# Kernel tuning notes

Measured on AMD Instinct MI355X. Metric: run time of the kernel, lower is better.

The kernel has to match this reference:

```python
import jax, jax.numpy as jnp
import numpy as np

B, L, C, D, H, NB, K = 8, 1024, 4, 64, 8, 2, 16  # batch, seq, conds, dim, heads, blocks, rbf centers

def _ln(x, s, b):
    m = x.mean(-1, keepdims=True)
    v = x.var(-1, keepdims=True)
    return (x - m) / jnp.sqrt(v + 1e-6) * s + b

def setup_inputs() -> dict:
    key = jax.random.key(0)
    ks = jax.random.split(key, 24)
    rn = lambda i, shape, sc=0.02: jax.random.normal(ks[i], shape, jnp.float32) * sc
    inp = {}
    inp['z'] = jax.random.normal(ks[0], (B, L), jnp.float32)
    inp['conditionals'] = jax.random.normal(ks[1], (C,), jnp.float32)
    inp['s'] = jnp.sort(jax.random.uniform(ks[2], (L,), jnp.float32))
    inp['embed'] = rn(3, (L, 2 * D - (C + 1)))  # positional id embedding table
    # input MLP([4D, D]) with gelu
    inp['Win1'] = rn(4, (2 * D, 4 * D)); inp['bin1'] = jnp.zeros((4 * D,), jnp.float32)
    inp['Win2'] = rn(5, (4 * D, D));     inp['bin2'] = jnp.zeros((D,), jnp.float32)
    # per-block (leading dim NB) transformer params
    inp['ln1_s'] = jnp.ones((NB, D), jnp.float32); inp['ln1_b'] = jnp.zeros((NB, D), jnp.float32)
    inp['ln2_s'] = jnp.ones((NB, D), jnp.float32); inp['ln2_b'] = jnp.zeros((NB, D), jnp.float32)
    inp['Wq'] = rn(6, (NB, D, 2 * D)); inp['bq'] = jnp.zeros((NB, 2 * D), jnp.float32)
    inp['Wk'] = rn(7, (NB, D, 2 * D)); inp['bk'] = jnp.zeros((NB, 2 * D), jnp.float32)
    inp['Wv'] = rn(8, (NB, D, 2 * D)); inp['bv'] = jnp.zeros((NB, 2 * D), jnp.float32)
    inp['Wo'] = rn(9, (NB, 2 * D, D)); inp['bo'] = jnp.zeros((NB, D), jnp.float32)
    # RBF-network attention bias: features exp(-(d-c)^2/(2w^2)) -> linear to H heads
    inp['rbf_c'] = jnp.tile(jnp.linspace(-1.0, 1.0, K, dtype=jnp.float32)[None], (NB, 1))
    inp['rbf_logw'] = jnp.full((NB, K), -1.0, jnp.float32)
    inp['rbf_w'] = rn(10, (NB, K, H), 0.1); inp['rbf_b'] = jnp.zeros((NB, H), jnp.float32)
    # FFN MLP([4D, D])
    inp['W1'] = rn(11, (NB, D, 4 * D)); inp['b1'] = jnp.zeros((NB, 4 * D), jnp.float32)
    inp['W2'] = rn(12, (NB, 4 * D, D)); inp['b2'] = jnp.zeros((NB, D), jnp.float32)
    # head MLP([4D, D, 1])
    inp['Wh1'] = rn(13, (D, 4 * D)); inp['bh1'] = jnp.zeros((4 * D,), jnp.float32)
    inp['Wh2'] = rn(14, (4 * D, D)); inp['bh2'] = jnp.zeros((D,), jnp.float32)
    inp['Wh3'] = rn(15, (D, 1));     inp['bh3'] = jnp.zeros((1,), jnp.float32)
    return inp

def reference(z, conditionals, s, embed, Win1, bin1, Win2, bin2,
              ln1_s, ln1_b, ln2_s, ln2_b, Wq, bq, Wk, bk, Wv, bv, Wo, bo,
              rbf_c, rbf_logw, rbf_w, rbf_b, W1, b1, W2, b2,
              Wh1, bh1, Wh2, bh2, Wh3, bh3):
    Bn, Ln = z.shape
    Cn = conditionals.shape[0]
    Hn = rbf_w.shape[-1]
    dh = Wq.shape[-1] // Hn
    scale = 1.0 / jnp.sqrt(jnp.float32(dh))
    # cond_as_feats: [z, broadcast conditionals] -> (B, L, C+1); prepend ids embedding -> (B, L, 2D)
    feats = jnp.concatenate([
        jnp.broadcast_to(embed[None], (Bn,) + embed.shape),
        z[..., None],
        jnp.broadcast_to(conditionals[None, None, :], (Bn, Ln, Cn)),
    ], axis=-1)
    x = jax.nn.gelu(feats @ Win1 + bin1) @ Win2 + bin2  # (B, L, D)
    dist = s[:, None] - s[None, :]  # (L, L) pairwise query-key coordinate diff (same per batch)
    for i in range(Wq.shape[0]):
        h = _ln(x, ln1_s[i], ln1_b[i])
        q = (h @ Wq[i] + bq[i]).reshape(Bn, Ln, Hn, dh)
        k = (h @ Wk[i] + bk[i]).reshape(Bn, Ln, Hn, dh)
        v = (h @ Wv[i] + bv[i]).reshape(Bn, Ln, Hn, dh)
        scores = jnp.einsum('bqhd,bkhd->bhqk', q, k) * scale
        # RBF-network bias on pairwise distances, per head
        phi = jnp.exp(-(dist[..., None] - rbf_c[i]) ** 2 / (2.0 * jnp.exp(rbf_logw[i]) ** 2))  # (L, L, K)
        bias = jnp.einsum('qkf,fh->hqk', phi, rbf_w[i]) + rbf_b[i][:, None, None]  # (H, L, L)
        a = jax.nn.softmax(scores + bias[None], axis=-1)
        o = jnp.einsum('bhqk,bkhd->bqhd', a, v).reshape(Bn, Ln, Hn * dh)
        x = x + o @ Wo[i] + bo[i]
        h2 = _ln(x, ln2_s[i], ln2_b[i])
        x = x + jax.nn.gelu(h2 @ W1[i] + b1[i]) @ W2[i] + b2[i]
    hh = jax.nn.gelu(x @ Wh1 + bh1)
    hh = jax.nn.gelu(hh @ Wh2 + bh2)
    return hh @ Wh3 + bh3  # f_hat: (B, L, 1)
```

## Files before the change

kernel.cpp:

```cpp
#include <hip/hip_runtime.h>
#include <hip/hip_bf16.h>

#define BB   8
#define LL   1024
#define DD   64
#define D2   128
#define D4   256
#define HH   8
#define DH   16

typedef __attribute__((ext_vector_type(8))) short short8;
typedef __attribute__((ext_vector_type(4))) float floatx4;

#define OFF_WIN1   0
#define OFF_WIN2   65536
#define OFF_LAY0   98304
#define LAY_STRIDE 131072
#define OFF_WQ     0
#define OFF_WK     16384
#define OFF_WV     32768
#define OFF_WO     49152
#define OFF_W1     65536
#define OFF_W2     98304
#define OFF_WH1    360448
#define OFF_WH2    393216

__device__ __forceinline__ float gelu_tanh(float u) {
  float t = tanhf(0.7978845608028654f * (u + 0.044715f * u * u * u));
  return 0.5f * u * (1.0f + t);
}

__device__ __forceinline__ float wave_reduce_sum(float v) {
#pragma unroll
  for (int m = 32; m >= 1; m >>= 1) v += __shfl_xor(v, m, 64);
  return v;
}

__device__ __forceinline__ unsigned short f2bf(float x) {
  unsigned u = __float_as_uint(x);
  u += 0x7fffu + ((u >> 16) & 1u);
  return (unsigned short)(u >> 16);
}

__device__ __forceinline__ float bf2f(unsigned short x) {
  return __uint_as_float(((unsigned)x) << 16);
}

__device__ __forceinline__ void split_bf(float v, unsigned short& hi,
                                         unsigned short& lo) {
  hi = f2bf(v);
  lo = f2bf(v - bf2f(hi));
}

template <int K, int KP>
__device__ __forceinline__ floatx4 mfma_tile(
    const unsigned short* Ah, const unsigned short* Al,
    const unsigned short* __restrict__ Bh, const unsigned short* __restrict__ Bl,
    int lq, int quad, floatx4 C) {
#pragma unroll
  for (int kk = 0; kk < K; kk += 32) {
    short8 ah = *(const short8*)(Ah + lq * KP + kk + quad * 8);
    short8 al = *(const short8*)(Al + lq * KP + kk + quad * 8);
    short8 bh = *(const short8*)(Bh + lq * K + kk + quad * 8);
    short8 bl = *(const short8*)(Bl + lq * K + kk + quad * 8);
    C = __builtin_amdgcn_mfma_f32_16x16x32_bf16(ah, bh, C, 0, 0, 0);
    C = __builtin_amdgcn_mfma_f32_16x16x32_bf16(al, bh, C, 0, 0, 0);
    C = __builtin_amdgcn_mfma_f32_16x16x32_bf16(ah, bl, C, 0, 0, 0);
  }
  return C;
}

struct PrepArgs {
  const float* src[16];
  int Kd[16], Nd[16], dst[16], elems[16];
};

__global__ __launch_bounds__(256) void k_prep(PrepArgs a,
                                              unsigned short* __restrict__ arena) {
  int mid = blockIdx.y;
  int e = blockIdx.x * 256 + threadIdx.x;
  int KN = a.elems[mid];
  if (e >= KN) return;
  int K = a.Kd[mid], N = a.Nd[mid];
  int n = e / K, k = e - n * K;
  float wv = a.src[mid][k * N + n];
  unsigned short hi, lo;
  split_bf(wv, hi, lo);
  arena[a.dst[mid] + e] = hi;
  arena[a.dst[mid] + KN + e] = lo;
}

__global__ __launch_bounds__(256) void k_bias(
    const float* __restrict__ s, const float* __restrict__ rbf_c,
    const float* __restrict__ rbf_logw, const float* __restrict__ rbf_w,
    const float* __restrict__ rbf_b, unsigned short* __restrict__ biasT) {
  int lay = blockIdx.y;
  int id = blockIdx.x * 256 + threadIdx.x;
  int q = id >> 10, k = id & 1023;
  float dd = s[q] - s[k];
  float acc[8];
#pragma unroll
  for (int h = 0; h < 8; ++h) acc[h] = rbf_b[lay * 8 + h];
#pragma unroll 1
  for (int f = 0; f < 16; ++f) {
    float c = rbf_c[lay * 16 + f];
    float inv2w2 = 0.5f * __expf(-2.0f * rbf_logw[lay * 16 + f]);
    float e = dd - c;
    float ph = __expf(-e * e * inv2w2);
#pragma unroll
    for (int h = 0; h < 8; ++h)
      acc[h] = fmaf(ph, rbf_w[lay * 128 + f * 8 + h], acc[h]);
  }
  unsigned short* bT = biasT + (size_t)lay * 8 * 1024 * 1024;
#pragma unroll
  for (int h = 0; h < 8; ++h)
    bT[(size_t)(h * 1024 + q) * 1024 + k] = f2bf(acc[h]);
}

__device__ __forceinline__ void qkv_tail(
    const float* xl, unsigned short* Sh, unsigned short* Sl,
    const unsigned short* __restrict__ arena, int lay,
    const float* __restrict__ ln_s, const float* __restrict__ ln_b,
    const float* __restrict__ bq, const float* __restrict__ bk,
    const float* __restrict__ bv, unsigned short* __restrict__ qo,
    unsigned short* __restrict__ ko, unsigned short* __restrict__ voT,
    int tok0, int t) {
  int w = t >> 6, lane = t & 63;
  int lq = lane & 15, quad = lane >> 4;
  float ss = ln_s[lay * 64 + lane], sb = ln_b[lay * 64 + lane];
#pragma unroll
  for (int tk = 0; tk < 4; ++tk) {
    int tok = w * 4 + tk;
    float v = xl[tok * 64 + lane];
    float mean = wave_reduce_sum(v) * 0.015625f;
    float d = v - mean;
    float var = wave_reduce_sum(d * d) * 0.015625f;
    float hv = d * rsqrtf(var + 1e-6f) * ss + sb;
    unsigned short hi, lo;
    split_bf(hv, hi, lo);
    Sh[tok * 72 + lane] = hi;
    Sl[tok * 72 + lane] = lo;
  }
  __syncthreads();
  int b = tok0 >> 10, l0 = tok0 & 1023;
#pragma unroll 1
  for (int mat = 0; mat < 3; ++mat) {
    const unsigned short* Bh =
        arena + OFF_LAY0 + lay * LAY_STRIDE + mat * 16384;
    const unsigned short* Bl = Bh + 8192;
    const float* bias = (mat == 0 ? bq : mat == 1 ? bk : bv) + lay * 128;
#pragma unroll
    for (int j = 0; j < 2; ++j) {
      int tl = w + j * 4;
      int n = tl * 16 + lq;
      float bb = bias[n];
      floatx4 C = {bb, bb, bb, bb};
      C = mfma_tile<64, 72>(Sh, Sl, Bh + tl * 16 * 64, Bl + tl * 16 * 64,
                            lq, quad, C);
      if (mat < 2) {
        unsigned short* outp = (mat == 0 ? qo : ko);
        size_t basea = ((size_t)(b * 8 + tl) * 1024 + l0 + quad * 4) * 16 + lq;
#pragma unroll
        for (int r = 0; r < 4; ++r)
          outp[basea + (size_t)r * 16] = f2bf(C[r]);
      } else {
        size_t basev = ((size_t)(b * 8 + tl) * 16 + lq) * 1024 + l0 + quad * 4;
#pragma unroll
        for (int r = 0; r < 4; ++r)
          voT[basev + r] = f2bf(C[r]);
      }
    }
  }
}

__global__ __launch_bounds__(256) void k_in_qkv(
    const float* __restrict__ embed, const float* __restrict__ z,
    const float* __restrict__ cond, const unsigned short* __restrict__ arena,
    const float* __restrict__ bin1, const float* __restrict__ bin2,
    float* __restrict__ x, const float* __restrict__ ln1_s,
    const float* __restrict__ ln1_b, const float* __restrict__ bq,
    const float* __restrict__ bk, const float* __restrict__ bv,
    unsigned short* __restrict__ qo, unsigned short* __restrict__ ko,
    unsigned short* __restrict__ voT) {
  __shared__ __align__(16) unsigned short Ah[16 * 136], Al[16 * 136];
  __shared__ __align__(16) unsigned short Hh[16 * 264], Hl[16 * 264];
  __shared__ __align__(16) unsigned short Sh[16 * 72], Sl[16 * 72];
  __shared__ float xl[16 * 64];
  int t = threadIdx.x, w = t >> 6, lane = t & 63;
  int lq = lane & 15, quad = lane >> 4;
  int tok0 = blockIdx.x * 16;
  for (int idx = t; idx < 2048; idx += 256) {
    int tok = idx >> 7, dim = idx & 127;
    int bl = tok0 + tok, l = bl & (LL - 1);
    float v;
    if (dim < 123) v = embed[l * 123 + dim];
    else if (dim == 123) v = z[bl];
    else v = cond[dim - 124];
    unsigned short hi, lo;
    split_bf(v, hi, lo);
    Ah[tok * 136 + dim] = hi;
    Al[tok * 136 + dim] = lo;
  }
  __syncthreads();
  const unsigned short* B1h = arena + OFF_WIN1;
  const unsigned short* B1l = B1h + 32768;
#pragma unroll
  for (int j = 0; j < 4; ++j) {
    int tl = w * 4 + j, n = tl * 16 + lq;
    float bb = bin1[n];
    floatx4 C = {bb, bb, bb, bb};
    C = mfma_tile<128, 136>(Ah, Al, B1h + tl * 16 * 128, B1l + tl * 16 * 128,
                            lq, quad, C);
#pragma unroll
    for (int r = 0; r < 4; ++r) {
      float g = gelu_tanh(C[r]);
      unsigned short hi, lo;
      split_bf(g, hi, lo);
      Hh[(quad * 4 + r) * 264 + n] = hi;
      Hl[(quad * 4 + r) * 264 + n] = lo;
    }
  }
  __syncthreads();
  const unsigned short* B2h = arena + OFF_WIN2;
  const unsigned short* B2l = B2h + 16384;
  {
    int n = w * 16 + lq;
    float bb = bin2[n];
    floatx4 C = {bb, bb, bb, bb};
    C = mfma_tile<256, 264>(Hh, Hl, B2h + w * 16 * 256, B2l + w * 16 * 256,
                            lq, quad, C);
#pragma unroll
    for (int r = 0; r < 4; ++r) {
      int m = quad * 4 + r;
      x[(size_t)(tok0 + m) * 64 + n] = C[r];
      xl[m * 64 + n] = C[r];
    }
  }
  __syncthreads();
  qkv_tail(xl, Sh, Sl, arena, 0, ln1_s, ln1_b, bq, bk, bv,
           qo, ko, voT, tok0, t);
}

__global__ __launch_bounds__(256) void k_attn(
    const unsigned short* __restrict__ qg, const unsigned short* __restrict__ kg,
    const unsigned short* __restrict__ vgT, const unsigned short* __restrict__ biasT,
    float* __restrict__ og) {
  __shared__ __align__(16) unsigned short Kl[64 * 32];
  __shared__ __align__(16) unsigned short VT[16 * 72];
  __shared__ __align__(16) unsigned short Pl[4][16 * 72];
  __shared__ __align__(16) unsigned short Bch[64 * 72];
  int t = threadIdx.x, w = t >> 6, lane = t & 63;
  int lq = lane & 15, quad = lane >> 4;
  int bid = blockIdx.x;
  int b = bid >> 7, h = (bid >> 4) & 7, qblk = bid & 15;
  int q0w = qblk * 64 + w * 16;
  size_t bh = (size_t)(b * 8 + h) * 1024;
  size_t bh16 = (size_t)(b * 8 + h) * 16;

  ((uint4*)Kl)[t] = uint4{0, 0, 0, 0};

  short8 Qb = {};
  if (quad < 2)
    Qb = *(const short8*)(qg + (bh + q0w + lq) * 16 + quad * 8);

  float m = -1e30f, l = 0.0f;
  floatx4 O = {0.0f, 0.0f, 0.0f, 0.0f};

  int key = t >> 2, dp = (t & 3) * 4;
  int drow = t >> 4, vcol = (t & 15) * 4;
  int qrow = t >> 2, bcol = (t & 3) * 16;
  const unsigned short* kgp = kg + (bh + key) * 16 + dp;
  const unsigned short* vgp = vgT + (bh16 + drow) * 1024 + vcol;
  const unsigned short* bgp =
      biasT + ((size_t)(h * 1024 + qblk * 64 + qrow)) * 1024 + bcol;

  uint2 kpre = *(const uint2*)(kgp);
  uint2 vpre = *(const uint2*)(vgp);
  uint4 bpre0 = *(const uint4*)(bgp);
  uint4 bpre1 = *(const uint4*)(bgp + 8);

#pragma unroll 1
  for (int kc = 0; kc < 1024; kc += 64) {
    __syncthreads();
    *(uint2*)(Kl + key * 32 + dp) = kpre;
    *(uint2*)(VT + drow * 72 + vcol) = vpre;
    *(uint4*)(Bch + qrow * 72 + bcol) = bpre0;
    *(uint4*)(Bch + qrow * 72 + bcol + 8) = bpre1;
    __syncthreads();
    if (kc + 64 < 1024) {
      kpre = *(const uint2*)(kgp + (size_t)(kc + 64) * 16);
      vpre = *(const uint2*)(vgp + (kc + 64));
      bpre0 = *(const uint4*)(bgp + (kc + 64));
      bpre1 = *(const uint4*)(bgp + (kc + 64) + 8);
    }
    float s[16];
#pragma unroll
    for (int tile = 0; tile < 4; ++tile) {
      short8 A = *(const short8*)(Kl + (tile * 16 + lq) * 32 + quad * 8);
      floatx4 c = {0.0f, 0.0f, 0.0f, 0.0f};
      c = __builtin_amdgcn_mfma_f32_16x16x32_bf16(A, Qb, c, 0, 0, 0);
      ushort4 bb = *(const ushort4*)(Bch + (w * 16 + lq) * 72 +
                                     tile * 16 + quad * 4);
      s[tile * 4 + 0] = fmaf(c[0], 0.25f, bf2f(bb.x));
      s[tile * 4 + 1] = fmaf(c[1], 0.25f, bf2f(bb.y));
      s[tile * 4 + 2] = fmaf(c[2], 0.25f, bf2f(bb.z));
      s[tile * 4 + 3] = fmaf(c[3], 0.25f, bf2f(bb.w));
    }
    float cm = s[0];
#pragma unroll
    for (int i = 1; i < 16; ++i) cm = fmaxf(cm, s[i]);
    cm = fmaxf(cm, __shfl_xor(cm, 16, 64));
    cm = fmaxf(cm, __shfl_xor(cm, 32, 64));
    float mnew = fmaxf(m, cm);
    float alpha = __expf(m - mnew);
    float p[16], psum = 0.0f;
#pragma unroll
    for (int i = 0; i < 16; ++i) {
      p[i] = __expf(s[i] - mnew);
      psum += p[i];
    }
    psum += __shfl_xor(psum, 16, 64);
    psum += __shfl_xor(psum, 32, 64);
    l = l * alpha + psum;
    m = mnew;
    unsigned short* pw = &Pl[w][lq * 72];
#pragma unroll
    for (int tile = 0; tile < 4; ++tile) {
      uint2 pk;
      pk.x = (unsigned)f2bf(p[tile * 4 + 0]) | ((unsigned)f2bf(p[tile * 4 + 1]) << 16);
      pk.y = (unsigned)f2bf(p[tile * 4 + 2]) | ((unsigned)f2bf(p[tile * 4 + 3]) << 16);
      *(uint2*)(pw + tile * 16 + quad * 4) = pk;
    }
    asm volatile("s_waitcnt lgkmcnt(0)" ::: "memory");
#pragma unroll
    for (int r = 0; r < 4; ++r) {
      int idx = (quad * 4 + r) * 4;
      float ar = __uint_as_float(
          __builtin_amdgcn_ds_bpermute(idx, __float_as_uint(alpha)));
      O[r] *= ar;
    }
#pragma unroll
    for (int i = 0; i < 2; ++i) {
      short8 Pa = *(const short8*)(pw + i * 32 + quad * 8);
      short8 Vb = *(const short8*)(&VT[lq * 72 + i * 32 + quad * 8]);
      O = __builtin_amdgcn_mfma_f32_16x16x32_bf16(Pa, Vb, O, 0, 0, 0);
    }
  }
  float linv = 1.0f / l;
#pragma unroll
  for (int r = 0; r < 4; ++r) {
    int idx = (quad * 4 + r) * 4;
    float lr = __uint_as_float(
        __builtin_amdgcn_ds_bpermute(idx, __float_as_uint(linv)));
    og[((size_t)(b * 1024 + q0w + quad * 4 + r)) * 128 + h * 16 + lq] = O[r] * lr;
  }
}

__device__ __forceinline__ void pf_body(
    const float* __restrict__ ob, const unsigned short* __restrict__ arena,
    const float* __restrict__ bo, float* __restrict__ x,
    const float* __restrict__ ln_s, const float* __restrict__ ln_b,
    const float* __restrict__ b1, const float* __restrict__ b2, int lay,
    unsigned short* Ah, unsigned short* Al, unsigned short* Sh,
    unsigned short* Sl, unsigned short* Hh, unsigned short* Hl, float* xl,
    int tok0, int t, bool write_x) {
  int w = t >> 6, lane = t & 63;
  int lq = lane & 15, quad = lane >> 4;
  const unsigned short* labase = arena + OFF_LAY0 + lay * LAY_STRIDE;
  for (int idx = t * 4; idx < 2048; idx += 1024) {
    int row = idx >> 7, col = idx & 127;
    float4 v = *(const float4*)(ob + (size_t)(tok0 + row) * 128 + col);
    unsigned short h0, e0, h1, e1, h2, e2, h3, e3;
    split_bf(v.x, h0, e0); split_bf(v.y, h1, e1);
    split_bf(v.z, h2, e2); split_bf(v.w, h3, e3);
    unsigned* ph = (unsigned*)(Ah + row * 136 + col);
    ph[0] = (unsigned)h0 | ((unsigned)h1 << 16);
    ph[1] = (unsigned)h2 | ((unsigned)h3 << 16);
    unsigned* pl = (unsigned*)(Al + row * 136 + col);
    pl[0] = (unsigned)e0 | ((unsigned)e1 << 16);
    pl[1] = (unsigned)e2 | ((unsigned)e3 << 16);
  }
  __syncthreads();
  {
    const unsigned short* Bh = labase + OFF_WO;
    const unsigned short* Bl = Bh + 8192;
    int n = w * 16 + lq;
    float bb = bo[lay * 64 + n];
    floatx4 C = {bb, bb, bb, bb};
    C = mfma_tile<128, 136>(Ah, Al, Bh + w * 16 * 128, Bl + w * 16 * 128,
                            lq, quad, C);
#pragma unroll
    for (int r = 0; r < 4; ++r) {
      int m = quad * 4 + r;
      xl[m * 64 + n] = x[(size_t)(tok0 + m) * 64 + n] + C[r];
    }
  }
  __syncthreads();
  {
    float ss = ln_s[lay * 64 + lane], sb = ln_b[lay * 64 + lane];
#pragma unroll
    for (int tk = 0; tk < 4; ++tk) {
      int tok = w * 4 + tk;
      float v = xl[tok * 64 + lane];
      float mean = wave_reduce_sum(v) * 0.015625f;
      float d = v - mean;
      float var = wave_reduce_sum(d * d) * 0.015625f;
      float hv = d * rsqrtf(var + 1e-6f) * ss + sb;
      unsigned short hi, lo;
      split_bf(hv, hi, lo);
      Sh[tok * 72 + lane] = hi;
      Sl[tok * 72 + lane] = lo;
    }
  }
  __syncthreads();
  {
    const unsigned short* Bh = labase + OFF_W1;
    const unsigned short* Bl = Bh + 16384;
#pragma unroll
    for (int j = 0; j < 4; ++j) {
      int tl = w * 4 + j, n = tl * 16 + lq;
      float bb = b1[lay * 256 + n];
      floatx4 C = {bb, bb, bb, bb};
      C = mfma_tile<64, 72>(Sh, Sl, Bh + tl * 16 * 64, Bl + tl * 16 * 64,
                            lq, quad, C);
#pragma unroll
      for (int r = 0; r < 4; ++r) {
        float g = gelu_tanh(C[r]);
        unsigned short hi, lo;
        split_bf(g, hi, lo);
        Hh[(quad * 4 + r) * 264 + n] = hi;
        Hl[(quad * 4 + r) * 264 + n] = lo;
      }
    }
  }
  __syncthreads();
  {
    const unsigned short* Bh = labase + OFF_W2;
    const unsigned short* Bl = Bh + 16384;
    int n = w * 16 + lq;
    float bb = b2[lay * 64 + n];
    floatx4 C = {bb, bb, bb, bb};
    C = mfma_tile<256, 264>(Hh, Hl, Bh + w * 16 * 256, Bl + w * 16 * 256,
                            lq, quad, C);
#pragma unroll
    for (int r = 0; r < 4; ++r) {
      int m = quad * 4 + r;
      float xv = xl[m * 64 + n] + C[r];
      xl[m * 64 + n] = xv;
      if (write_x) x[(size_t)(tok0 + m) * 64 + n] = xv;
    }
  }
  __syncthreads();
}

__global__ __launch_bounds__(256) void k_pf_qkv(
    const float* __restrict__ ob, const unsigned short* __restrict__ arena,
    const float* __restrict__ bo, float* __restrict__ x,
    const float* __restrict__ ln2_s, const float* __restrict__ ln2_b,
    const float* __restrict__ b1, const float* __restrict__ b2, int lay,
    const float* __restrict__ ln1_s, const float* __restrict__ ln1_b,
    const float* __restrict__ bq, const float* __restrict__ bk,
    const float* __restrict__ bv, unsigned short* __restrict__ qo,
    unsigned short* __restrict__ ko, unsigned short* __restrict__ voT) {
  __shared__ __align__(16) unsigned short Ah[16 * 136], Al[16 * 136];
  __shared__ __align__(16) unsigned short Sh[16 * 72], Sl[16 * 72];
  __shared__ __align__(16) unsigned short Hh[16 * 264], Hl[16 * 264];
  __shared__ float xl[16 * 64];
  int t = threadIdx.x;
  int tok0 = blockIdx.x * 16;
  pf_body(ob, arena, bo, x, ln2_s, ln2_b, b1, b2, lay,
          Ah, Al, Sh, Sl, Hh, Hl, xl, tok0, t, true);
  qkv_tail(xl, Sh, Sl, arena, lay + 1, ln1_s, ln1_b, bq, bk, bv,
           qo, ko, voT, tok0, t);
}

__global__ __launch_bounds__(256) void k_pf_head(
    const float* __restrict__ ob, const unsigned short* __restrict__ arena,
    const float* __restrict__ bo, float* __restrict__ x,
    const float* __restrict__ ln2_s, const float* __restrict__ ln2_b,
    const float* __restrict__ b1, const float* __restrict__ b2, int lay,
    const float* __restrict__ bh1, const float* __restrict__ bh2,
    const float* __restrict__ Wh3, const float* __restrict__ bh3,
    float* __restrict__ out) {
  __shared__ __align__(16) unsigned short Ah[16 * 136], Al[16 * 136];
  __shared__ __align__(16) unsigned short Sh[16 * 72], Sl[16 * 72];
  __shared__ __align__(16) unsigned short Hh[16 * 264], Hl[16 * 264];
  __shared__ float xl[16 * 64];
  int t = threadIdx.x, w = t >> 6, lane = t & 63;
  int lq = lane & 15, quad = lane >> 4;
  int tok0 = blockIdx.x * 16;
  pf_body(ob, arena, bo, x, ln2_s, ln2_b, b1, b2, lay,
          Ah, Al, Sh, Sl, Hh, Hl, xl, tok0, t, false);
#pragma unroll
  for (int tk = 0; tk < 4; ++tk) {
    int tok = w * 4 + tk;
    unsigned short hi, lo;
    split_bf(xl[tok * 64 + lane], hi, lo);
    Sh[tok * 72 + lane] = hi;
    Sl[tok * 72 + lane] = lo;
  }
  __syncthreads();
  {
    const unsigned short* Bh = arena + OFF_WH1;
    const unsigned short* Bl = Bh + 16384;
#pragma unroll
    for (int j = 0; j < 4; ++j) {
      int tl = w * 4 + j, n = tl * 16 + lq;
      float bb = bh1[n];
      floatx4 C = {bb, bb, bb, bb};
      C = mfma_tile<64, 72>(Sh, Sl, Bh + tl * 16 * 64, Bl + tl * 16 * 64,
                            lq, quad, C);
#pragma unroll
      for (int r = 0; r < 4; ++r) {
        float g = gelu_tanh(C[r]);
        unsigned short hi, lo;
        split_bf(g, hi, lo);
        Hh[(quad * 4 + r) * 264 + n] = hi;
        Hl[(quad * 4 + r) * 264 + n] = lo;
      }
    }
  }
  __syncthreads();
  {
    const unsigned short* Bh = arena + OFF_WH2;
    const unsigned short* Bl = Bh + 16384;
    int n = w * 16 + lq;
    float bb = bh2[n];
    floatx4 C = {bb, bb, bb, bb};
    C = mfma_tile<256, 264>(Hh, Hl, Bh + w * 16 * 256, Bl + w * 16 * 256,
                            lq, quad, C);
    __syncthreads();
#pragma unroll
    for (int r = 0; r < 4; ++r)
      xl[(quad * 4 + r) * 64 + n] = gelu_tanh(C[r]);
  }
  __syncthreads();
  float wv3 = Wh3[lane];
#pragma unroll
  for (int tk = 0; tk < 4; ++tk) {
    int tok = w * 4 + tk;
    float v = xl[tok * 64 + lane] * wv3;
    float sum = wave_reduce_sum(v);
    if (lane == 0) out[tok0 + tok] = sum + bh3[0];
  }
}

extern "C" void kernel_launch(void* const* d_in, const int* in_sizes, int n_in,
                              void* d_out, int out_size, void* d_ws, size_t ws_size,
                              hipStream_t stream) {
  const float* z      = (const float*)d_in[0];
  const float* cond   = (const float*)d_in[1];
  const float* s      = (const float*)d_in[2];
  const float* embed  = (const float*)d_in[3];
  const float* Win1   = (const float*)d_in[4];
  const float* bin1   = (const float*)d_in[5];
  const float* Win2   = (const float*)d_in[6];
  const float* bin2   = (const float*)d_in[7];
  const float* ln1_s  = (const float*)d_in[8];
  const float* ln1_b  = (const float*)d_in[9];
  const float* ln2_s  = (const float*)d_in[10];
  const float* ln2_b  = (const float*)d_in[11];
  const float* Wq     = (const float*)d_in[12];
  const float* bq     = (const float*)d_in[13];
  const float* Wk     = (const float*)d_in[14];
  const float* bk     = (const float*)d_in[15];
  const float* Wv     = (const float*)d_in[16];
  const float* bv     = (const float*)d_in[17];
  const float* Wo     = (const float*)d_in[18];
  const float* bo     = (const float*)d_in[19];
  const float* rbf_c  = (const float*)d_in[20];
  const float* rbf_lw = (const float*)d_in[21];
  const float* rbf_w  = (const float*)d_in[22];
  const float* rbf_b  = (const float*)d_in[23];
  const float* W1     = (const float*)d_in[24];
  const float* b1     = (const float*)d_in[25];
  const float* W2     = (const float*)d_in[26];
  const float* b2     = (const float*)d_in[27];
  const float* Wh1    = (const float*)d_in[28];
  const float* bh1    = (const float*)d_in[29];
  const float* Wh2    = (const float*)d_in[30];
  const float* bh2    = (const float*)d_in[31];
  const float* Wh3    = (const float*)d_in[32];
  const float* bh3    = (const float*)d_in[33];

  char* base = (char*)d_ws;
  float*          x     = (float*)(base);
  unsigned short* qb    = (unsigned short*)(base + (2u << 20));
  unsigned short* kb    = (unsigned short*)(base + (4u << 20));
  unsigned short* vbT   = (unsigned short*)(base + (6u << 20));
  float*          ob    = (float*)(base + (8u << 20));
  unsigned short* biasT = (unsigned short*)(base + (12u << 20));
  unsigned short* arena = (unsigned short*)(base + (48u << 20));

  PrepArgs pa;
  auto set = [&](int i, const float* sp, int K, int N, int dst) {
    pa.src[i] = sp; pa.Kd[i] = K; pa.Nd[i] = N; pa.dst[i] = dst;
    pa.elems[i] = K * N;
  };
  set(0, Win1, 128, 256, OFF_WIN1);
  set(1, Win2, 256, 64, OFF_WIN2);
  for (int lay = 0; lay < 2; ++lay) {
    int lb = OFF_LAY0 + lay * LAY_STRIDE;
    set(2 + lay * 6, Wq + lay * 8192, 64, 128, lb + OFF_WQ);
    set(3 + lay * 6, Wk + lay * 8192, 64, 128, lb + OFF_WK);
    set(4 + lay * 6, Wv + lay * 8192, 64, 128, lb + OFF_WV);
    set(5 + lay * 6, Wo + lay * 8192, 128, 64, lb + OFF_WO);
    set(6 + lay * 6, W1 + lay * 16384, 64, 256, lb + OFF_W1);
    set(7 + lay * 6, W2 + lay * 16384, 256, 64, lb + OFF_W2);
  }
  set(14, Wh1, 64, 256, OFF_WH1);
  set(15, Wh2, 256, 64, OFF_WH2);

  k_prep<<<dim3(128, 16), 256, 0, stream>>>(pa, arena);
  k_bias<<<dim3(4096, 2), 256, 0, stream>>>(s, rbf_c, rbf_lw, rbf_w, rbf_b, biasT);
  k_in_qkv<<<512, 256, 0, stream>>>(embed, z, cond, arena, bin1, bin2, x,
                                    ln1_s, ln1_b, bq, bk, bv, qb, kb, vbT);
  k_attn<<<1024, 256, 0, stream>>>(qb, kb, vbT, biasT, ob);
  k_pf_qkv<<<512, 256, 0, stream>>>(ob, arena, bo, x, ln2_s, ln2_b, b1, b2, 0,
                                    ln1_s, ln1_b, bq, bk, bv, qb, kb, vbT);
  k_attn<<<1024, 256, 0, stream>>>(qb, kb, vbT,
                                   biasT + (size_t)8 * 1024 * 1024, ob);
  k_pf_head<<<512, 256, 0, stream>>>(ob, arena, bo, x, ln2_s, ln2_b, b1, b2, 1,
                                     bh1, bh2, Wh3, bh3, (float*)d_out);
}
```

Measured before the change: 275.4 us.

## Double query rows per attention block and merge prep and bias kernels

Each attention wave now processes 32 query rows (two 16-row tiles) instead of 16. Every K/V chunk staged in shared memory is therefore reused across twice as many queries, and the grid shrinks from 1024 to 512 blocks. The weight-prep and RBF-bias kernels are merged into one launch to save a kernel launch. In exchange, each wave uses more registers and shared memory, and the smaller grid on 256 CUs may leave some compute units underused.

After: 283.9 us. 1.03x slower.

```diff
diff --git a/kernel.cpp b/kernel.cpp
--- a/kernel.cpp
+++ b/kernel.cpp
@@ -75,27 +75,29 @@
   int Kd[16], Nd[16], dst[16], elems[16];
 };
 
-__global__ __launch_bounds__(256) void k_prep(PrepArgs a,
-                                              unsigned short* __restrict__ arena) {
-  int mid = blockIdx.y;
-  int e = blockIdx.x * 256 + threadIdx.x;
-  int KN = a.elems[mid];
-  if (e >= KN) return;
-  int K = a.Kd[mid], N = a.Nd[mid];
-  int n = e / K, k = e - n * K;
-  float wv = a.src[mid][k * N + n];
-  unsigned short hi, lo;
-  split_bf(wv, hi, lo);
-  arena[a.dst[mid] + e] = hi;
-  arena[a.dst[mid] + KN + e] = lo;
-}
-
-__global__ __launch_bounds__(256) void k_bias(
+__global__ __launch_bounds__(256) void k_prep_bias(
+    PrepArgs a, unsigned short* __restrict__ arena,
     const float* __restrict__ s, const float* __restrict__ rbf_c,
     const float* __restrict__ rbf_logw, const float* __restrict__ rbf_w,
     const float* __restrict__ rbf_b, unsigned short* __restrict__ biasT) {
-  int lay = blockIdx.y;
-  int id = blockIdx.x * 256 + threadIdx.x;
+  int bid = blockIdx.x, t = threadIdx.x;
+  if (bid < 2048) {
+    int mid = bid >> 7;
+    int e = (bid & 127) * 256 + t;
+    int KN = a.elems[mid];
+    if (e >= KN) return;
+    int K = a.Kd[mid], N = a.Nd[mid];
+    int n = e / K, k = e - n * K;
+    float wv = a.src[mid][k * N + n];
+    unsigned short hi, lo;
+    split_bf(wv, hi, lo);
+    arena[a.dst[mid] + e] = hi;
+    arena[a.dst[mid] + KN + e] = lo;
+    return;
+  }
+  int rem = bid - 2048;
+  int lay = rem >> 12;
+  int id = (rem & 4095) * 256 + t;
   int q = id >> 10, k = id & 1023;
   float dd = s[q] - s[k];
   float acc[8];
@@ -247,112 +249,136 @@
     float* __restrict__ og) {
   __shared__ __align__(16) unsigned short Kl[64 * 32];
   __shared__ __align__(16) unsigned short VT[16 * 72];
-  __shared__ __align__(16) unsigned short Pl[4][16 * 72];
-  __shared__ __align__(16) unsigned short Bch[64 * 72];
+  __shared__ __align__(16) unsigned short Pl[4][32 * 72];
+  __shared__ __align__(16) unsigned short Bch[128 * 72];
   int t = threadIdx.x, w = t >> 6, lane = t & 63;
   int lq = lane & 15, quad = lane >> 4;
   int bid = blockIdx.x;
-  int b = bid >> 7, h = (bid >> 4) & 7, qblk = bid & 15;
-  int q0w = qblk * 64 + w * 16;
+  int b = bid >> 6, h = (bid >> 3) & 7, qblk = bid & 7;
+  int q0w = qblk * 128 + w * 32;
   size_t bh = (size_t)(b * 8 + h) * 1024;
   size_t bh16 = (size_t)(b * 8 + h) * 16;
 
   ((uint4*)Kl)[t] = uint4{0, 0, 0, 0};
 
-  short8 Qb = {};
-  if (quad < 2)
-    Qb = *(const short8*)(qg + (bh + q0w + lq) * 16 + quad * 8);
-
-  float m = -1e30f, l = 0.0f;
-  floatx4 O = {0.0f, 0.0f, 0.0f, 0.0f};
+  short8 Qb[2] = {{}, {}};
+  if (quad < 2) {
+#pragma unroll
+    for (int u = 0; u < 2; ++u)
+      Qb[u] = *(const short8*)(qg + (bh + q0w + u * 16 + lq) * 16 + quad * 8);
+  }
+
+  float m[2] = {-1e30f, -1e30f}, l[2] = {0.0f, 0.0f};
+  floatx4 O[2] = {{0.0f, 0.0f, 0.0f, 0.0f}, {0.0f, 0.0f, 0.0f, 0.0f}};
 
   int key = t >> 2, dp = (t & 3) * 4;
   int drow = t >> 4, vcol = (t & 15) * 4;
-  int qrow = t >> 2, bcol = (t & 3) * 16;
+  int qrow = t >> 1, bcol = (t & 1) * 32;
   const unsigned short* kgp = kg + (bh + key) * 16 + dp;
   const unsigned short* vgp = vgT + (bh16 + drow) * 1024 + vcol;
   const unsigned short* bgp =
-      biasT + ((size_t)(h * 1024 + qblk * 64 + qrow)) * 1024 + bcol;
+      biasT + ((size_t)(h * 1024 + qblk * 128 + qrow)) * 1024 + bcol;
 
   uint2 kpre = *(const uint2*)(kgp);
   uint2 vpre = *(const uint2*)(vgp);
   uint4 bpre0 = *(const uint4*)(bgp);
   uint4 bpre1 = *(const uint4*)(bgp + 8);
+  uint4 bpre2 = *(const uint4*)(bgp + 16);
+  uint4 bpre3 = *(const uint4*)(bgp + 24);
 
 #pragma unroll 1
   for (int kc = 0; kc < 1024; kc += 64) {
     __syncthreads();
     *(uint2*)(Kl + key * 32 + dp) = kpre;
     *(uint2*)(VT + drow * 72 + vcol) = vpre;
-    *(uint4*)(Bch + qrow * 72 + bcol) = bpre0;
-    *(uint4*)(Bch + qrow * 72 + bcol + 8) = bpre1;
+    {
+      unsigned short* bp = Bch + qrow * 72 + bcol;
+      *(uint4*)(bp) = bpre0;
+      *(uint4*)(bp + 8) = bpre1;
+      *(uint4*)(bp + 16) = bpre2;
+      *(uint4*)(bp + 24) = bpre3;
+    }
     __syncthreads();
     if (kc + 64 < 1024) {
       kpre = *(const uint2*)(kgp + (size_t)(kc + 64) * 16);
       vpre = *(const uint2*)(vgp + (kc + 64));
       bpre0 = *(const uint4*)(bgp + (kc + 64));
       bpre1 = *(const uint4*)(bgp + (kc + 64) + 8);
-    }
-    float s[16];
+      bpre2 = *(const uint4*)(bgp + (kc + 64) + 16);
+      bpre3 = *(const uint4*)(bgp + (kc + 64) + 24);
+    }
+    float s[2][16];
 #pragma unroll
     for (int tile = 0; tile < 4; ++tile) {
       short8 A = *(const short8*)(Kl + (tile * 16 + lq) * 32 + quad * 8);
-      floatx4 c = {0.0f, 0.0f, 0.0f, 0.0f};
-      c = __builtin_amdgcn_mfma_f32_16x16x32_bf16(A, Qb, c, 0, 0, 0);
-      ushort4 bb = *(const ushort4*)(Bch + (w * 16 + lq) * 72 +
-                                     tile * 16 + quad * 4);
-      s[tile * 4 + 0] = fmaf(c[0], 0.25f, bf2f(bb.x));
-      s[tile * 4 + 1] = fmaf(c[1], 0.25f, bf2f(bb.y));
-      s[tile * 4 + 2] = fmaf(c[2], 0.25f, bf2f(bb.z));
-      s[tile * 4 + 3] = fmaf(c[3], 0.25f, bf2f(bb.w));
-    }
-    float cm = s[0];
-#pragma unroll
-    for (int i = 1; i < 16; ++i) cm = fmaxf(cm, s[i]);
-    cm = fmaxf(cm, __shfl_xor(cm, 16, 64));
-    cm = fmaxf(cm, __shfl_xor(cm, 32, 64));
-    float mnew = fmaxf(m, cm);
-    float alpha = __expf(m - mnew);
-    float p[16], psum = 0.0f;
-#pragma unroll
-    for (int i = 0; i < 16; ++i) {
-      p[i] = __expf(s[i] - mnew);
-      psum += p[i];
-    }
-    psum += __shfl_xor(psum, 16, 64);
-    psum += __shfl_xor(psum, 32, 64);
-    l = l * alpha + psum;
-    m = mnew;
-    unsigned short* pw = &Pl[w][lq * 72];
-#pragma unroll
-    for (int tile = 0; tile < 4; ++tile) {
-      uint2 pk;
-      pk.x = (unsigned)f2bf(p[tile * 4 + 0]) | ((unsigned)f2bf(p[tile * 4 + 1]) << 16);
-      pk.y = (unsigned)f2bf(p[tile * 4 + 2]) | ((unsigned)f2bf(p[tile * 4 + 3]) << 16);
-      *(uint2*)(pw + tile * 16 + quad * 4) = pk;
-    }
-    asm volatile("s_waitcnt lgkmcnt(0)" ::: "memory");
+#pragma unroll
+      for (int u = 0; u < 2; ++u) {
+        floatx4 c = {0.0f, 0.0f, 0.0f, 0.0f};
+        c = __builtin_amdgcn_mfma_f32_16x16x32_bf16(A, Qb[u], c, 0, 0, 0);
+        ushort4 bb = *(const ushort4*)(Bch + (w * 32 + u * 16 + lq) * 72 +
+                                       tile * 16 + quad * 4);
+        s[u][tile * 4 + 0] = fmaf(c[0], 0.25f, bf2f(bb.x));
+        s[u][tile * 4 + 1] = fmaf(c[1], 0.25f, bf2f(bb.y));
+        s[u][tile * 4 + 2] = fmaf(c[2], 0.25f, bf2f(bb.z));
+        s[u][tile * 4 + 3] = fmaf(c[3], 0.25f, bf2f(bb.w));
+      }
+    }
+#pragma unroll
+    for (int u = 0; u < 2; ++u) {
+      float cm = s[u][0];
+#pragma unroll
+      for (int i = 1; i < 16; ++i) cm = fmaxf(cm, s[u][i]);
+      cm = fmaxf(cm, __shfl_xor(cm, 16, 64));
+      cm = fmaxf(cm, __shfl_xor(cm, 32, 64));
+      float mnew = fmaxf(m[u], cm);
+      float alpha = __expf(m[u] - mnew);
+      float p[16], psum = 0.0f;
+#pragma unroll
+      for (int i = 0; i < 16; ++i) {
+        p[i] = __expf(s[u][i] - mnew);
+        psum += p[i];
+      }
+      psum += __shfl_xor(psum, 16, 64);
+      psum += __shfl_xor(psum, 32, 64);
+      l[u] = l[u] * alpha + psum;
+      m[u] = mnew;
+      unsigned short* pw = &Pl[w][(u * 16 + lq) * 72];
+#pragma unroll
+      for (int tile = 0; tile < 4; ++tile) {
+        uint2 pk;
+        pk.x = (unsigned)f2bf(p[tile * 4 + 0]) |
+               ((unsigned)f2bf(p[tile * 4 + 1]) << 16);
+        pk.y = (unsigned)f2bf(p[tile * 4 + 2]) |
+               ((unsigned)f2bf(p[tile * 4 + 3]) << 16);
+        *(uint2*)(pw + tile * 16 + quad * 4) = pk;
+      }
+      asm volatile("s_waitcnt lgkmcnt(0)" ::: "memory");
+#pragma unroll
+      for (int r = 0; r < 4; ++r) {
+        int idx = (quad * 4 + r) * 4;
+        float ar = __uint_as_float(
+            __builtin_amdgcn_ds_bpermute(idx, __float_as_uint(alpha)));
+        O[u][r] *= ar;
+      }
+#pragma unroll
+      for (int i = 0; i < 2; ++i) {
+        short8 Pa = *(const short8*)(&Pl[w][(u * 16 + lq) * 72 + i * 32 + quad * 8]);
+        short8 Vb = *(const short8*)(&VT[lq * 72 + i * 32 + quad * 8]);
+        O[u] = __builtin_amdgcn_mfma_f32_16x16x32_bf16(Pa, Vb, O[u], 0, 0, 0);
+      }
+    }
+  }
+#pragma unroll
+  for (int u = 0; u < 2; ++u) {
+    float linv = 1.0f / l[u];
 #pragma unroll
     for (int r = 0; r < 4; ++r) {
       int idx = (quad * 4 + r) * 4;
-      float ar = __uint_as_float(
-          __builtin_amdgcn_ds_bpermute(idx, __float_as_uint(alpha)));
-      O[r] *= ar;
-    }
-#pragma unroll
-    for (int i = 0; i < 2; ++i) {
-      short8 Pa = *(const short8*)(pw + i * 32 + quad * 8);
-      short8 Vb = *(const short8*)(&VT[lq * 72 + i * 32 + quad * 8]);
-      O = __builtin_amdgcn_mfma_f32_16x16x32_bf16(Pa, Vb, O, 0, 0, 0);
-    }
-  }
-  float linv = 1.0f / l;
-#pragma unroll
-  for (int r = 0; r < 4; ++r) {
-    int idx = (quad * 4 + r) * 4;
-    float lr = __uint_as_float(
-        __builtin_amdgcn_ds_bpermute(idx, __float_as_uint(linv)));
-    og[((size_t)(b * 1024 + q0w + quad * 4 + r)) * 128 + h * 16 + lq] = O[r] * lr;
+      float lr = __uint_as_float(
+          __builtin_amdgcn_ds_bpermute(idx, __float_as_uint(linv)));
+      og[((size_t)(b * 1024 + q0w + u * 16 + quad * 4 + r)) * 128 + h * 16 + lq] =
+          O[u][r] * lr;
+    }
   }
 }
 
@@ -611,15 +637,15 @@
   set(14, Wh1, 64, 256, OFF_WH1);
   set(15, Wh2, 256, 64, OFF_WH2);
 
-  k_prep<<<dim3(128, 16), 256, 0, stream>>>(pa, arena);
-  k_bias<<<dim3(4096, 2), 256, 0, stream>>>(s, rbf_c, rbf_lw, rbf_w, rbf_b, biasT);
+  k_prep_bias<<<2048 + 8192, 256, 0, stream>>>(pa, arena, s, rbf_c, rbf_lw,
+                                               rbf_w, rbf_b, biasT);
   k_in_qkv<<<512, 256, 0, stream>>>(embed, z, cond, arena, bin1, bin2, x,
                                     ln1_s, ln1_b, bq, bk, bv, qb, kb, vbT);
-  k_attn<<<1024, 256, 0, stream>>>(qb, kb, vbT, biasT, ob);
+  k_attn<<<512, 256, 0, stream>>>(qb, kb, vbT, biasT, ob);
   k_pf_qkv<<<512, 256, 0, stream>>>(ob, arena, bo, x, ln2_s, ln2_b, b1, b2, 0,
                                     ln1_s, ln1_b, bq, bk, bv, qb, kb, vbT);
-  k_attn<<<1024, 256, 0, stream>>>(qb, kb, vbT,
-                                   biasT + (size_t)8 * 1024 * 1024, ob);
+  k_attn<<<512, 256, 0, stream>>>(qb, kb, vbT,
+                                  biasT + (size_t)8 * 1024 * 1024, ob);
   k_pf_head<<<512, 256, 0, stream>>>(ob, arena, bo, x, ln2_s, ln2_b, b1, b2, 1,
                                      bh1, bh2, Wh3, bh3, (float*)d_out);
 }
```
